# Kernel tuning notes

Measured on AMD Instinct MI355X. Metric: run time of the kernel, lower is better.

Reference implementation:

```python
import jax, jax.numpy as jnp
import numpy as np

N_NODES = 50000
EMB = 256
HEADS = 2
N_BASE_EDGES = 100000


def setup_inputs() -> dict:
    key = jax.random.key(0)
    ks = jax.random.split(key, 12)
    x = jax.random.normal(ks[0], (N_NODES, EMB), dtype=jnp.float32)
    # bipartite edges: sources in left half, targets in right half -> no self-loops
    src = jax.random.randint(ks[1], (N_BASE_EDGES,), 0, N_NODES // 2)
    dst = jax.random.randint(ks[2], (N_BASE_EDGES,), N_NODES // 2, N_NODES)
    edge_index = jnp.stack([src, dst]).astype(jnp.int64)
    hd = EMB // HEADS
    s = 0.02
    params = {
        "Wkqv": jax.random.normal(ks[3], (EMB, 3 * EMB), dtype=jnp.float32) * s,
        "bkqv": jnp.zeros((3 * EMB,), dtype=jnp.float32),
        "W1": jax.random.normal(ks[4], (2 * hd, hd), dtype=jnp.float32) * s,
        "b1": jnp.zeros((hd,), dtype=jnp.float32),
        "W2": jax.random.normal(ks[5], (hd, 1), dtype=jnp.float32) * s,
        "b2": jnp.zeros((1,), dtype=jnp.float32),
        "Wout": jax.random.normal(ks[6], (EMB, EMB), dtype=jnp.float32) * s,
        "bout": jnp.zeros((EMB,), dtype=jnp.float32),
    }
    return {"x": x, "edge_index": edge_index, **params}


def reference(x, edge_index, Wkqv, bkqv, W1, b1, W2, b2, Wout, bout):
    N, emb = x.shape
    H = HEADS
    hd = emb // H
    # MetaGNNNoEdgeAttr.forward preprocessing: make undirected + self loops.
    # Input is bipartite (no self-loops), so remove_self_loops is a no-op.
    ei = jnp.concatenate([edge_index, edge_index[::-1]], axis=1)
    loops = jnp.arange(N, dtype=edge_index.dtype)
    src = jnp.concatenate([ei[0], loops])  # j (message source)
    dst = jnp.concatenate([ei[1], loops])  # i (message target / softmax index)

    # single GNN layer (n_layers=1)
    kqv = x @ Wkqv + bkqv  # [N, 3*emb]
    q = kqv[dst, :emb].reshape(-1, H, hd)                                  # [E,H,hd]
    k = kqv[src, emb:2 * emb].reshape(-1, H, hd) / jnp.sqrt(jnp.float32(hd))
    v = kqv[src, 2 * emb:].reshape(-1, H, hd)

    h = jax.nn.relu(jnp.concatenate([k, q], axis=-1) @ W1 + b1)  # [E,H,hd]
    a = (h @ W2 + b2).squeeze(-1)                                # [E,H]

    # segment softmax over destination nodes (every node has a self-loop)
    m = jax.ops.segment_max(a, dst, num_segments=N)              # [N,H]
    ex = jnp.exp(a - m[dst])
    s = jax.ops.segment_sum(ex, dst, num_segments=N)             # [N,H]
    alpha = ex / (s[dst] + 1e-16)                                # [E,H]

    msg = (alpha[..., None] * v).reshape(-1, emb) @ Wout + bout  # [E,emb]
    out = jax.ops.segment_sum(msg, dst, num_segments=N)          # [N,emb]
    return jax.nn.relu(out) + x
```

## Files before the change

### kernel.cpp

```cpp
#include <hip/hip_runtime.h>
#include <hip/hip_bf16.h>

#define EMB 256

typedef __bf16 bf16_t;
typedef __attribute__((ext_vector_type(8))) __bf16 bf16x8;
typedef __attribute__((ext_vector_type(4))) __bf16 bf16x4;
typedef __attribute__((ext_vector_type(4))) float floatx4;

__device__ __forceinline__ int eidx(const int* __restrict__ p, int is64, long long k){
  return is64 ? p[2*k] : p[(int)k];
}
__device__ __forceinline__ void async_load16(const void* g, void* l){
  __builtin_amdgcn_global_load_lds(
      (const __attribute__((address_space(1))) unsigned int*)g,
      (__attribute__((address_space(3))) unsigned int*)l,
      16, 0, 0);
}
__device__ __forceinline__ float4 cvt4(bf16x4 v){
  return make_float4((float)v.x, (float)v.y, (float)v.z, (float)v.w);
}

__global__ void detect_kernel(const int* __restrict__ ei, int* __restrict__ flag){
  int z = (ei[1]==0) + (ei[3]==0) + (ei[5]==0) + (ei[7]==0);
  *flag = (z == 4) ? 1 : 0;
}

__global__ void cvt_x_kernel(const float* __restrict__ x, bf16_t* __restrict__ xb, int n4){
  int t = blockIdx.x*blockDim.x + threadIdx.x;
  if (t >= n4) return;
  const float4 v = *(const float4*)(x + (size_t)t*4);
  bf16x4 o = { (bf16_t)v.x, (bf16_t)v.y, (bf16_t)v.z, (bf16_t)v.w };
  *(bf16x4*)(xb + (size_t)t*4) = o;
}

__global__ void prep_weights(const float* __restrict__ Wkqv, const float* __restrict__ bkqv,
                             const float* __restrict__ W1,
                             bf16_t* __restrict__ WcombT, float* __restrict__ bcomb){
  int n = blockIdx.x * blockDim.x + threadIdx.x;
  int c = blockIdx.y;
  if (n >= 768) return;
  const float rs = rsqrtf(128.0f);
  bool isBias = (c == 256);
  const float* arow = isBias ? bkqv : (Wkqv + (size_t)c*768);
  float val;
  if (n < 256){
    int h = n >> 7, d = n & 127;
    float s = 0.f;
    for (int t = 0; t < 128; ++t)
      s = fmaf(arow[h*128 + t], W1[(size_t)(128 + t)*128 + d], s);
    val = s;
  } else {
    int r = n - 256;
    int h = r >> 8, t8 = r & 255;
    int g = t8 >> 3, half = (t8 >> 2) & 1, dd = t8 & 3;
    int d = g*4 + dd;
    if (half == 0){
      float s = 0.f;
      for (int t = 0; t < 128; ++t)
        s = fmaf(arow[256 + h*128 + t], W1[(size_t)t*128 + d], s);
      val = s * rs;
    } else {
      val = arow[512 + h*128 + d];
    }
  }
  if (isBias) bcomb[n] = val;
  else        WcombT[(size_t)n*256 + c] = (bf16_t)val;
}

__global__ void prep_wout(const float* __restrict__ W, bf16_t* __restrict__ Wt){
  int t = blockIdx.x*blockDim.x + threadIdx.x;
  int n = t & 255, c = t >> 8;
  Wt[(size_t)n*256 + c] = (bf16_t)W[(size_t)c*256 + n];
}

__global__ void deg_kernel(const int* __restrict__ ei, const int* __restrict__ flag,
                           int* __restrict__ deg, int E0, int Nn){
  int t = blockIdx.x*blockDim.x + threadIdx.x;
  if (t >= 2*E0) return;
  int is64 = *flag;
  int i = (t < E0) ? eidx(ei,is64,(long long)E0+t) : eidx(ei,is64,t-E0);
  i = min(max(i,0), Nn-1);
  atomicAdd(deg + i, 1);
}

__global__ __launch_bounds__(1024) void scan_kernel(const int* __restrict__ deg,
                                                    int* __restrict__ off, int N){
  __shared__ int wsum[16];
  __shared__ int carry_s;
  int tid = threadIdx.x, lane = tid & 63, w = tid >> 6;
  if (tid == 0) carry_s = 0;
  __syncthreads();
  for (int base = 0; base < N; base += 1024){
    int carry = carry_s;
    int v = (base + tid < N) ? (deg[base + tid] + 1) : 0;
    int incl = v;
    #pragma unroll
    for (int o = 1; o < 64; o <<= 1){
      int t = __shfl_up(incl, o, 64);
      if (lane >= o) incl += t;
    }
    if (lane == 63) wsum[w] = incl;
    __syncthreads();
    if (w == 0 && lane < 16){
      int sv = wsum[lane];
      #pragma unroll
      for (int o = 1; o < 16; o <<= 1){
        int t = __shfl_up(sv, o, 64);
        if (lane >= o) sv += t;
      }
      wsum[lane] = sv;
    }
    __syncthreads();
    int wpref = (w == 0) ? 0 : wsum[w-1];
    if (base + tid < N) off[base + tid] = carry + wpref + incl - v;
    __syncthreads();
    if (tid == 1023) carry_s = carry + wsum[15];
    __syncthreads();
  }
  if (threadIdx.x == 0) off[N] = carry_s;
}

__global__ void scatter_kernel(const int* __restrict__ ei, const int* __restrict__ flag,
                               const int* __restrict__ off, int* __restrict__ cursor,
                               int* __restrict__ bj, int E0, int Nn){
  int e = blockIdx.x*blockDim.x + threadIdx.x;
  int E = 2*E0 + Nn;
  if (e >= E) return;
  int is64 = *flag;
  int j, i;
  if (e < E0){ j = eidx(ei,is64,e); i = eidx(ei,is64,(long long)E0+e); }
  else if (e < 2*E0){ int t = e - E0; i = eidx(ei,is64,t); j = eidx(ei,is64,(long long)E0+t); }
  else { i = j = e - 2*E0; }
  i = min(max(i,0), Nn-1); j = min(max(j,0), Nn-1);
  int pos = atomicAdd(cursor + i, 1);
  bj[off[i] + pos] = j;
}

template<int MODE, typename OutT>
__global__ __launch_bounds__(256) void mfma_gemm(
    const bf16_t* __restrict__ A, const bf16_t* __restrict__ Bt,
    const float* __restrict__ bias, OutT* __restrict__ C,
    int M, int N,
    const int* __restrict__ deg, const float* __restrict__ xres)
{
  __shared__ bf16_t As[2][128*32];
  __shared__ bf16_t Bs[2][128*32];
  const int tid = threadIdx.x;
  const int wave = tid >> 6, lane = tid & 63;
  const int row16 = lane & 15, quad = lane >> 4;

  const int nn = N >> 7;
  const int bid = blockIdx.x;
  const int strip = bid / (8*nn);
  const int inner = bid % (8*nn);
  const int m0 = (strip*8 + (inner & 7)) * 128;
  const int n0 = (inner >> 3) * 128;
  const int wm = (wave >> 1) * 64, wn = (wave & 1) * 64;

  const int f0 = wave*2, f1 = wave*2 + 1;
  const int gm0 = min(m0 + f0*16 + row16, M-1);
  const int gm1 = min(m0 + f1*16 + row16, M-1);
  const int gn0 = n0 + f0*16 + row16;
  const int gn1 = n0 + f1*16 + row16;

  async_load16(A  + (size_t)gm0*256 + quad*8, (char*)As[0] + f0*1024);
  async_load16(A  + (size_t)gm1*256 + quad*8, (char*)As[0] + f1*1024);
  async_load16(Bt + (size_t)gn0*256 + quad*8, (char*)Bs[0] + f0*1024);
  async_load16(Bt + (size_t)gn1*256 + quad*8, (char*)Bs[0] + f1*1024);

  floatx4 acc[4][4];
  #pragma unroll
  for (int a=0;a<4;++a)
    #pragma unroll
    for (int b=0;b<4;++b) acc[a][b] = (floatx4){0.f,0.f,0.f,0.f};

  #pragma unroll
  for (int kt = 0; kt < 8; ++kt){
    const int cur = kt & 1, nxt = cur ^ 1;
    const int k1 = (kt+1)*32;

    __syncthreads();

    if (kt < 7){
      async_load16(A  + (size_t)gm0*256 + k1 + quad*8, (char*)As[nxt] + f0*1024);
      async_load16(A  + (size_t)gm1*256 + k1 + quad*8, (char*)As[nxt] + f1*1024);
      async_load16(Bt + (size_t)gn0*256 + k1 + quad*8, (char*)Bs[nxt] + f0*1024);
      async_load16(Bt + (size_t)gn1*256 + k1 + quad*8, (char*)Bs[nxt] + f1*1024);
    }

    bf16x8 af[4], bfr[4];
    #pragma unroll
    for (int t = 0; t < 4; ++t){
      af[t]  = *(const bf16x8*)((const char*)As[cur] + ((wm>>4)+t)*1024 + lane*16);
      bfr[t] = *(const bf16x8*)((const char*)Bs[cur] + ((wn>>4)+t)*1024 + lane*16);
    }
    #pragma unroll
    for (int mt=0;mt<4;++mt)
      #pragma unroll
      for (int nt=0;nt<4;++nt)
        acc[mt][nt] = __builtin_amdgcn_mfma_f32_16x16x32_bf16(bfr[nt], af[mt], acc[mt][nt], 0,0,0);
  }

  float4 b4[4];
  #pragma unroll
  for (int nt=0;nt<4;++nt)
    b4[nt] = *(const float4*)(bias + n0 + wn + nt*16 + quad*4);

  #pragma unroll
  for (int mt=0;mt<4;++mt){
    const int m = m0 + wm + mt*16 + row16;
    if (m >= M) continue;
    const float dg = (MODE==1) ? (float)(deg[m]+1) : 0.f;
    #pragma unroll
    for (int nt=0;nt<4;++nt){
      const int nb = n0 + wn + nt*16 + quad*4;
      if (MODE == 0){
        bf16x4 o = { (bf16_t)(acc[mt][nt][0] + b4[nt].x),
                     (bf16_t)(acc[mt][nt][1] + b4[nt].y),
                     (bf16_t)(acc[mt][nt][2] + b4[nt].z),
                     (bf16_t)(acc[mt][nt][3] + b4[nt].w) };
        *(bf16x4*)((bf16_t*)C + (size_t)m*N + nb) = o;
      } else {
        const float4 xr = *(const float4*)(xres + (size_t)m*N + nb);
        float4 o;
        o.x = fmaxf(acc[mt][nt][0] + dg*b4[nt].x, 0.f) + xr.x;
        o.y = fmaxf(acc[mt][nt][1] + dg*b4[nt].y, 0.f) + xr.y;
        o.z = fmaxf(acc[mt][nt][2] + dg*b4[nt].z, 0.f) + xr.z;
        o.w = fmaxf(acc[mt][nt][3] + dg*b4[nt].w, 0.f) + xr.w;
        *(float4*)((float*)C + (size_t)m*N + nb) = o;
      }
    }
  }
}

__global__ __launch_bounds__(256) void fused_attn_kernel(
    const bf16_t* __restrict__ P, const int* __restrict__ bj, const int* __restrict__ off,
    const float* __restrict__ b1, const float* __restrict__ W2, const float* __restrict__ b2,
    bf16_t* __restrict__ aggb, int Nn)
{
  int i = blockIdx.x * (blockDim.x >> 6) + (threadIdx.x >> 6);
  if (i >= Nn) return;
  int lane = threadIdx.x & 63;
  int h = lane >> 5, g = lane & 31, d = g * 4;

  const float4 qv  = cvt4(*(const bf16x4*)(P + (size_t)i*768 + h*128 + d));
  const float4 b1v = *(const float4*)(b1 + d);
  const float4 w2v = *(const float4*)(W2 + d);
  const float b2v  = b2[0];

  float m = -3.0e38f, s = 0.f;
  float4 acc = make_float4(0.f,0.f,0.f,0.f);
  int s0 = off[i], s1 = off[i+1];
  for (int t = s0; t < s1; ++t){
    int j = bj[t];
    bf16x8 kvv = *(const bf16x8*)(P + (size_t)j*768 + 256 + h*256 + g*8);
    float kx = (float)kvv[0], ky = (float)kvv[1], kz = (float)kvv[2], kw = (float)kvv[3];
    float vx = (float)kvv[4], vy = (float)kvv[5], vz = (float)kvv[6], vw = (float)kvv[7];
    float p = fmaxf(qv.x+kx+b1v.x, 0.f)*w2v.x
            + fmaxf(qv.y+ky+b1v.y, 0.f)*w2v.y
            + fmaxf(qv.z+kz+b1v.z, 0.f)*w2v.z
            + fmaxf(qv.w+kw+b1v.w, 0.f)*w2v.w;
    #pragma unroll
    for (int o = 16; o >= 1; o >>= 1)
      p += __shfl_xor(p, o, 64);
    float a = p + b2v;
    float mn = fmaxf(m, a);
    float sc = __expf(m - mn);
    float e  = __expf(a - mn);
    s = s*sc + e;
    acc.x = fmaf(acc.x, sc, e*vx);
    acc.y = fmaf(acc.y, sc, e*vy);
    acc.z = fmaf(acc.z, sc, e*vz);
    acc.w = fmaf(acc.w, sc, e*vw);
    m = mn;
  }
  float inv = 1.f / (s + 1e-16f);
  bf16x4 ob = { (bf16_t)(acc.x*inv), (bf16_t)(acc.y*inv), (bf16_t)(acc.z*inv), (bf16_t)(acc.w*inv) };
  *(bf16x4*)(aggb + (size_t)i*256 + h*128 + d) = ob;
}

extern "C" void kernel_launch(void* const* d_in, const int* in_sizes, int n_in,
                              void* d_out, int out_size, void* d_ws, size_t ws_size,
                              hipStream_t stream)
{
  const float* x     = (const float*)d_in[0];
  const int*   ei    = (const int*)d_in[1];
  const float* Wkqv  = (const float*)d_in[2];
  const float* bkqv  = (const float*)d_in[3];
  const float* W1    = (const float*)d_in[4];
  const float* b1    = (const float*)d_in[5];
  const float* W2    = (const float*)d_in[6];
  const float* b2    = (const float*)d_in[7];
  const float* Wout  = (const float*)d_in[8];
  const float* bout  = (const float*)d_in[9];
  float* out = (float*)d_out;

  const int N  = in_sizes[0] / EMB;
  const int E0 = in_sizes[1] / 2;
  const int E  = 2*E0 + N;

  float* base = (float*)d_ws;
  bf16_t* WcombT = (bf16_t*)base;
  float*  bcomb  = base + 98304;
  bf16_t* WoutT  = (bf16_t*)(base + 98304 + 768);
  bf16_t* xb     = (bf16_t*)(base + 131840);
  bf16_t* Pb     = (bf16_t*)(base + 131840 + 6400000);
  bf16_t* aggb   = (bf16_t*)(Pb + (size_t)N*768);
  int* deg       = (int*)(aggb + (size_t)N*256);
  int* cursor    = deg + N;
  int* flag      = cursor + N;
  int* off       = flag + 1;
  int* bj        = off + (N+1);

  hipMemsetAsync(deg, 0, (size_t)2*N*sizeof(int), stream);

  detect_kernel<<<1,1,0,stream>>>(ei, flag);
  cvt_x_kernel<<<((N*EMB/4)+255)/256,256,0,stream>>>(x, xb, N*EMB/4);
  prep_weights<<<dim3(3,257),256,0,stream>>>(Wkqv, bkqv, W1, WcombT, bcomb);
  prep_wout<<<256,256,0,stream>>>(Wout, WoutT);

  deg_kernel<<<(2*E0+255)/256,256,0,stream>>>(ei, flag, deg, E0, N);
  scan_kernel<<<1,1024,0,stream>>>(deg, off, N);
  scatter_kernel<<<(E+255)/256,256,0,stream>>>(ei, flag, off, cursor, bj, E0, N);

  const int nm8 = (((N+127)/128) + 7) & ~7;
  mfma_gemm<0, bf16_t><<<nm8*6,256,0,stream>>>(xb, WcombT, bcomb, Pb, N, 768, nullptr, nullptr);
  fused_attn_kernel<<<(N+3)/4,256,0,stream>>>(Pb, bj, off, b1, W2, b2, aggb, N);
  mfma_gemm<1, float><<<nm8*2,256,0,stream>>>(aggb, WoutT, bout, out, N, 256, deg, x);
}
```

Before: 339.8 us.

## Parallelize degree scan across blocks and unroll attention edge loop by four

The single-block serial prefix scan over node degrees becomes a three-kernel multi-block scan: per-block scan, a scan of block sums, then an add-back. Its temporary block sums live in the aggregation buffer before that buffer is written. The fused attention loop now handles four neighbor edges per iteration. It issues four independent K/V gathers and combines them with a single online-softmax rescale, which raises memory-level parallelism and cuts serial dependency chains. The cost is two extra kernel launches and wasted duplicate loads on the tail when the degree is not a multiple of four.

```diff
diff --git a/kernel.cpp b/kernel.cpp
--- a/kernel.cpp
+++ b/kernel.cpp
@@ -84,41 +84,67 @@
   atomicAdd(deg + i, 1);
 }
 
-__global__ __launch_bounds__(1024) void scan_kernel(const int* __restrict__ deg,
-                                                    int* __restrict__ off, int N){
+__global__ __launch_bounds__(1024) void scan1_kernel(const int* __restrict__ deg,
+                                                     int* __restrict__ off,
+                                                     int* __restrict__ bsum, int N){
   __shared__ int wsum[16];
-  __shared__ int carry_s;
   int tid = threadIdx.x, lane = tid & 63, w = tid >> 6;
-  if (tid == 0) carry_s = 0;
+  int i = blockIdx.x*1024 + tid;
+  int v = (i < N) ? (deg[i] + 1) : 0;
+  int incl = v;
+  #pragma unroll
+  for (int o = 1; o < 64; o <<= 1){
+    int t = __shfl_up(incl, o, 64);
+    if (lane >= o) incl += t;
+  }
+  if (lane == 63) wsum[w] = incl;
   __syncthreads();
-  for (int base = 0; base < N; base += 1024){
-    int carry = carry_s;
-    int v = (base + tid < N) ? (deg[base + tid] + 1) : 0;
-    int incl = v;
-    #pragma unroll
-    for (int o = 1; o < 64; o <<= 1){
-      int t = __shfl_up(incl, o, 64);
-      if (lane >= o) incl += t;
-    }
-    if (lane == 63) wsum[w] = incl;
-    __syncthreads();
-    if (w == 0 && lane < 16){
-      int sv = wsum[lane];
-      #pragma unroll
-      for (int o = 1; o < 16; o <<= 1){
-        int t = __shfl_up(sv, o, 64);
-        if (lane >= o) sv += t;
-      }
-      wsum[lane] = sv;
-    }
-    __syncthreads();
-    int wpref = (w == 0) ? 0 : wsum[w-1];
-    if (base + tid < N) off[base + tid] = carry + wpref + incl - v;
-    __syncthreads();
-    if (tid == 1023) carry_s = carry + wsum[15];
-    __syncthreads();
-  }
-  if (threadIdx.x == 0) off[N] = carry_s;
+  if (w == 0 && lane < 16){
+    int sv = wsum[lane];
+    #pragma unroll
+    for (int o = 1; o < 16; o <<= 1){
+      int t = __shfl_up(sv, o, 64);
+      if (lane >= o) sv += t;
+    }
+    wsum[lane] = sv;
+  }
+  __syncthreads();
+  int wpref = (w == 0) ? 0 : wsum[w-1];
+  if (i < N) off[i] = wpref + incl - v;
+  if (tid == 1023) bsum[blockIdx.x] = wpref + incl;
+}
+
+__global__ __launch_bounds__(1024) void scan2_kernel(int* __restrict__ bsum,
+                                                     int* __restrict__ off, int nb, int N){
+  __shared__ int wsum[16];
+  int tid = threadIdx.x, lane = tid & 63, w = tid >> 6;
+  int v = (tid < nb) ? bsum[tid] : 0;
+  int incl = v;
+  #pragma unroll
+  for (int o = 1; o < 64; o <<= 1){
+    int t = __shfl_up(incl, o, 64);
+    if (lane >= o) incl += t;
+  }
+  if (lane == 63) wsum[w] = incl;
+  __syncthreads();
+  if (w == 0 && lane < 16){
+    int sv = wsum[lane];
+    #pragma unroll
+    for (int o = 1; o < 16; o <<= 1){
+      int t = __shfl_up(sv, o, 64);
+      if (lane >= o) sv += t;
+    }
+    wsum[lane] = sv;
+  }
+  __syncthreads();
+  int wpref = (w == 0) ? 0 : wsum[w-1];
+  if (tid < nb) bsum[tid] = wpref + incl - v;
+  if (tid == 1023) off[N] = wpref + incl;
+}
+
+__global__ void scan3_kernel(int* __restrict__ off, const int* __restrict__ bsum, int N){
+  int i = blockIdx.x*256 + threadIdx.x;
+  if (i < N) off[i] += bsum[i >> 10];
 }
 
 __global__ void scatter_kernel(const int* __restrict__ ei, const int* __restrict__ flag,
@@ -234,6 +260,18 @@
   }
 }
 
+__device__ __forceinline__ float score4(bf16x8 kvv, float4 qv, float4 b1v, float4 w2v){
+  return fmaxf(qv.x+(float)kvv[0]+b1v.x, 0.f)*w2v.x
+       + fmaxf(qv.y+(float)kvv[1]+b1v.y, 0.f)*w2v.y
+       + fmaxf(qv.z+(float)kvv[2]+b1v.z, 0.f)*w2v.z
+       + fmaxf(qv.w+(float)kvv[3]+b1v.w, 0.f)*w2v.w;
+}
+__device__ __forceinline__ float hredux(float p){
+  #pragma unroll
+  for (int o = 16; o >= 1; o >>= 1)
+    p += __shfl_xor(p, o, 64);
+  return p;
+}
 __global__ __launch_bounds__(256) void fused_attn_kernel(
     const bf16_t* __restrict__ P, const int* __restrict__ bj, const int* __restrict__ off,
     const float* __restrict__ b1, const float* __restrict__ W2, const float* __restrict__ b2,
@@ -248,31 +286,42 @@
   const float4 b1v = *(const float4*)(b1 + d);
   const float4 w2v = *(const float4*)(W2 + d);
   const float b2v  = b2[0];
+  const bf16_t* __restrict__ Pkv = P + 256 + h*256 + g*8;
 
   float m = -3.0e38f, s = 0.f;
   float4 acc = make_float4(0.f,0.f,0.f,0.f);
-  int s0 = off[i], s1 = off[i+1];
-  for (int t = s0; t < s1; ++t){
-    int j = bj[t];
-    bf16x8 kvv = *(const bf16x8*)(P + (size_t)j*768 + 256 + h*256 + g*8);
-    float kx = (float)kvv[0], ky = (float)kvv[1], kz = (float)kvv[2], kw = (float)kvv[3];
-    float vx = (float)kvv[4], vy = (float)kvv[5], vz = (float)kvv[6], vw = (float)kvv[7];
-    float p = fmaxf(qv.x+kx+b1v.x, 0.f)*w2v.x
-            + fmaxf(qv.y+ky+b1v.y, 0.f)*w2v.y
-            + fmaxf(qv.z+kz+b1v.z, 0.f)*w2v.z
-            + fmaxf(qv.w+kw+b1v.w, 0.f)*w2v.w;
-    #pragma unroll
-    for (int o = 16; o >= 1; o >>= 1)
-      p += __shfl_xor(p, o, 64);
-    float a = p + b2v;
-    float mn = fmaxf(m, a);
-    float sc = __expf(m - mn);
-    float e  = __expf(a - mn);
-    s = s*sc + e;
-    acc.x = fmaf(acc.x, sc, e*vx);
-    acc.y = fmaf(acc.y, sc, e*vy);
-    acc.z = fmaf(acc.z, sc, e*vz);
-    acc.w = fmaf(acc.w, sc, e*vw);
+  const int s0 = off[i], s1 = off[i+1], s1m1 = s1 - 1;
+
+  for (int t = s0; t < s1; t += 4){
+    const int cnt = s1 - t;
+    const int jA = bj[t];
+    const int jB = bj[min(t+1, s1m1)];
+    const int jC = bj[min(t+2, s1m1)];
+    const int jD = bj[min(t+3, s1m1)];
+    const bf16x8 kA = *(const bf16x8*)(Pkv + (size_t)jA*768);
+    const bf16x8 kB = *(const bf16x8*)(Pkv + (size_t)jB*768);
+    const bf16x8 kC = *(const bf16x8*)(Pkv + (size_t)jC*768);
+    const bf16x8 kD = *(const bf16x8*)(Pkv + (size_t)jD*768);
+    float pA = hredux(score4(kA, qv, b1v, w2v));
+    float pB = hredux(score4(kB, qv, b1v, w2v));
+    float pC = hredux(score4(kC, qv, b1v, w2v));
+    float pD = hredux(score4(kD, qv, b1v, w2v));
+    const float aA = pA + b2v;
+    const float aB = (cnt > 1) ? pB + b2v : -3.0e38f;
+    const float aC = (cnt > 2) ? pC + b2v : -3.0e38f;
+    const float aD = (cnt > 3) ? pD + b2v : -3.0e38f;
+    const float amax = fmaxf(fmaxf(aA, aB), fmaxf(aC, aD));
+    const float mn = fmaxf(m, amax);
+    const float sc = __expf(m - mn);
+    const float eA = __expf(aA - mn);
+    const float eB = __expf(aB - mn);
+    const float eC = __expf(aC - mn);
+    const float eD = __expf(aD - mn);
+    s = s*sc + ((eA + eB) + (eC + eD));
+    acc.x = acc.x*sc + ((eA*(float)kA[4] + eB*(float)kB[4]) + (eC*(float)kC[4] + eD*(float)kD[4]));
+    acc.y = acc.y*sc + ((eA*(float)kA[5] + eB*(float)kB[5]) + (eC*(float)kC[5] + eD*(float)kD[5]));
+    acc.z = acc.z*sc + ((eA*(float)kA[6] + eB*(float)kB[6]) + (eC*(float)kC[6] + eD*(float)kD[6]));
+    acc.w = acc.w*sc + ((eA*(float)kA[7] + eB*(float)kB[7]) + (eC*(float)kC[7] + eD*(float)kD[7]));
     m = mn;
   }
   float inv = 1.f / (s + 1e-16f);
@@ -312,6 +361,7 @@
   int* flag      = cursor + N;
   int* off       = flag + 1;
   int* bj        = off + (N+1);
+  int* bsum      = (int*)aggb;
 
   hipMemsetAsync(deg, 0, (size_t)2*N*sizeof(int), stream);
 
@@ -321,7 +371,10 @@
   prep_wout<<<256,256,0,stream>>>(Wout, WoutT);
 
   deg_kernel<<<(2*E0+255)/256,256,0,stream>>>(ei, flag, deg, E0, N);
-  scan_kernel<<<1,1024,0,stream>>>(deg, off, N);
+  const int nb = (N + 1023)/1024;
+  scan1_kernel<<<nb,1024,0,stream>>>(deg, off, bsum, N);
+  scan2_kernel<<<1,1024,0,stream>>>(bsum, off, nb, N);
+  scan3_kernel<<<(N+255)/256,256,0,stream>>>(off, bsum, N);
   scatter_kernel<<<(E+255)/256,256,0,stream>>>(ei, flag, off, cursor, bj, E0, N);
 
   const int nm8 = (((N+127)/128) + 7) & ~7;
```

Result: faster. 293.0 us (-13.8%).
